# Performance work log

Hardware: AMD Instinct MI355X
Metric: run time of the kernel (lower is better)

## Reference

```python
import jax, jax.numpy as jnp
import numpy as np

N_HEADS = 8
N_NODES = 100_000
DEG = 16
N_EDGES = N_NODES * DEG
IN_DIM = 256
OUT_DIM = 128


def setup_inputs() -> dict:
    key = jax.random.key(0)
    k1, k2, k3, k4 = jax.random.split(key, 4)
    X = jax.random.normal(k1, (N_NODES, IN_DIM), dtype=jnp.float32)
    weights = jax.random.normal(k2, (IN_DIM, OUT_DIM), dtype=jnp.float32) * (1.0 / np.sqrt(IN_DIM))
    attention_w = jax.random.normal(k3, (1, N_HEADS), dtype=jnp.float32) * 0.1
    # valid CSR with uniform degree DEG
    row_pointers = (jnp.arange(N_NODES + 1, dtype=jnp.int32) * DEG)
    column_index = jax.random.randint(k4, (N_EDGES,), 0, N_NODES, dtype=jnp.int32)
    # TC-GNN block bookkeeping tensors: kernel-schedule metadata, no effect on math
    blockPartition = jnp.zeros(((N_NODES + 15) // 16,), dtype=jnp.int32)
    edgeToColumn = jnp.zeros((N_EDGES,), dtype=jnp.int32)
    edgeToRow = jnp.zeros((N_EDGES,), dtype=jnp.int32)
    return {
        "X": X,
        "weights": weights,
        "attention_w": attention_w,
        "row_pointers": row_pointers,
        "column_index": column_index,
        "blockPartition": blockPartition,
        "edgeToColumn": edgeToColumn,
        "edgeToRow": edgeToRow,
    }


def reference(X, weights, attention_w, row_pointers, column_index,
              blockPartition, edgeToColumn, edgeToRow):
    n_nodes = X.shape[0]
    n_edges = column_index.shape[0]
    # dense projection: X_prime = X @ W  -> [n_nodes, out_dim]
    X_prime = X @ weights
    # CSR row id of each edge: row_ids[e] = r s.t. row_pointers[r] <= e < row_pointers[r+1]
    row_ids = jnp.searchsorted(row_pointers,
                               jnp.arange(n_edges, dtype=row_pointers.dtype),
                               side="right") - 1
    # SDDMM (GAcc.forward_ef): per-edge scalar feature = <X_prime[src], X_prime[dst]>
    dst = X_prime[column_index]                    # [E, out_dim]
    edge_feature = jnp.sum(X_prime[row_ids] * dst, axis=-1)  # [E]
    # edge_attentions = outer(edge_feature, attention_w) -> [n_heads, E];
    # aggregation kernel collapses heads: att_e = edge_feature_e * sum_h(w_h)
    att = edge_feature * jnp.sum(attention_w)      # [E]
    # attention-weighted SpMM (GAcc.forward_gat): scatter-add into destination rows
    out = jax.ops.segment_sum(att[:, None] * dst, row_ids, num_segments=n_nodes)
    return out
```

## Files before the change

kernel.cpp:

```cpp
#include <hip/hip_runtime.h>
#include <hip/hip_bf16.h>
#include <stdint.h>

#define N_NODES 100000
#define IN_DIM 256
#define OUT_DIM 128
#define DEG 16

typedef __bf16 bf16x8 __attribute__((ext_vector_type(8)));
typedef __bf16 bf16x4 __attribute__((ext_vector_type(4)));
typedef float f32x4 __attribute__((ext_vector_type(4)));

__global__ void prep_w_kernel(const float* __restrict__ W, __bf16* __restrict__ Wt) {
    const int j = blockIdx.x;
    const int k = threadIdx.x;
    Wt[j * IN_DIM + k] = (__bf16)W[k * OUT_DIM + j];
}

__global__ __launch_bounds__(256) void gemm_kernel(const float* __restrict__ X,
                                                   const __bf16* __restrict__ Wt,
                                                   __bf16* __restrict__ XP) {
    __shared__ __bf16 Alds[32][264];
    const int m0 = blockIdx.x * 32;
    const int t = threadIdx.x;

    {
        const int row = t >> 3;
        const int seg = (t & 7) * 32;
        const float* src = X + (size_t)(m0 + row) * IN_DIM + seg;
        #pragma unroll
        for (int i = 0; i < 8; ++i) {
            float4 v = *reinterpret_cast<const float4*>(src + i * 4);
            bf16x4 b;
            b[0] = (__bf16)v.x; b[1] = (__bf16)v.y; b[2] = (__bf16)v.z; b[3] = (__bf16)v.w;
            *reinterpret_cast<bf16x4*>(&Alds[row][seg + i * 4]) = b;
        }
    }
    __syncthreads();

    const int lane = t & 63;
    const int wave = t >> 6;
    const int n0 = wave * 32;
    const int lr = lane & 15;
    const int lg = lane >> 4;
    f32x4 acc[2][2] = {};

    const __bf16* wbase0 = Wt + (size_t)(n0 + lr) * IN_DIM;
    const __bf16* wbase1 = Wt + (size_t)(n0 + 16 + lr) * IN_DIM;

    #pragma unroll
    for (int kk = 0; kk < IN_DIM; kk += 32) {
        const int ko = kk + lg * 8;
        bf16x8 a0 = *reinterpret_cast<const bf16x8*>(&Alds[lr][ko]);
        bf16x8 a1 = *reinterpret_cast<const bf16x8*>(&Alds[16 + lr][ko]);
        bf16x8 b0 = *reinterpret_cast<const bf16x8*>(wbase0 + ko);
        bf16x8 b1 = *reinterpret_cast<const bf16x8*>(wbase1 + ko);
        acc[0][0] = __builtin_amdgcn_mfma_f32_16x16x32_bf16(a0, b0, acc[0][0], 0, 0, 0);
        acc[0][1] = __builtin_amdgcn_mfma_f32_16x16x32_bf16(a0, b1, acc[0][1], 0, 0, 0);
        acc[1][0] = __builtin_amdgcn_mfma_f32_16x16x32_bf16(a1, b0, acc[1][0], 0, 0, 0);
        acc[1][1] = __builtin_amdgcn_mfma_f32_16x16x32_bf16(a1, b1, acc[1][1], 0, 0, 0);
    }

    #pragma unroll
    for (int mi = 0; mi < 2; ++mi)
        #pragma unroll
        for (int ni = 0; ni < 2; ++ni)
            #pragma unroll
            for (int r = 0; r < 4; ++r) {
                const int row = m0 + mi * 16 + lg * 4 + r;
                const int col = n0 + ni * 16 + lr;
                XP[(size_t)row * OUT_DIM + col] = (__bf16)acc[mi][ni][r];
            }
}

__global__ __launch_bounds__(256) void gat_edge_kernel(const __bf16* __restrict__ XP,
                                                       const int* __restrict__ rp,
                                                       const int* __restrict__ ci,
                                                       const float* __restrict__ attw,
                                                       float* __restrict__ out) {
    const int lane = threadIdx.x & 63;
    const int row = blockIdx.x * 4 + (threadIdx.x >> 6);
    const int g = lane >> 4;
    const int sl = lane & 15;

    float s = 0.f;
    #pragma unroll
    for (int h = 0; h < 8; ++h) s += attw[h];

    float x[8];
    {
        uint4 xv = *reinterpret_cast<const uint4*>(XP + (size_t)row * OUT_DIM + sl * 8);
        const uint32_t* xw = reinterpret_cast<const uint32_t*>(&xv);
        #pragma unroll
        for (int i = 0; i < 4; ++i) {
            x[2 * i]     = __uint_as_float(xw[i] << 16);
            x[2 * i + 1] = __uint_as_float(xw[i] & 0xffff0000u);
        }
    }

    const int4 cv = reinterpret_cast<const int4*>(ci + (size_t)row * DEG)[g];
    const int c[4] = {cv.x, cv.y, cv.z, cv.w};

    uint4 dvu[4];
    #pragma unroll
    for (int j = 0; j < 4; ++j)
        dvu[j] = *reinterpret_cast<const uint4*>(XP + (size_t)c[j] * OUT_DIM + sl * 8);

    float d[4][8];
    #pragma unroll
    for (int j = 0; j < 4; ++j) {
        const uint32_t* dw = reinterpret_cast<const uint32_t*>(&dvu[j]);
        #pragma unroll
        for (int i = 0; i < 4; ++i) {
            d[j][2 * i]     = __uint_as_float(dw[i] << 16);
            d[j][2 * i + 1] = __uint_as_float(dw[i] & 0xffff0000u);
        }
    }

    float p[4];
    #pragma unroll
    for (int j = 0; j < 4; ++j) {
        float t0 = 0.f;
        #pragma unroll
        for (int i = 0; i < 8; ++i) t0 += x[i] * d[j][i];
        p[j] = t0;
    }
    #pragma unroll
    for (int off = 1; off <= 8; off <<= 1) {
        #pragma unroll
        for (int j = 0; j < 4; ++j) p[j] += __shfl_xor(p[j], off);
    }

    float acc[8] = {};
    #pragma unroll
    for (int j = 0; j < 4; ++j) {
        const float att = p[j] * s;
        #pragma unroll
        for (int i = 0; i < 8; ++i) acc[i] += att * d[j][i];
    }

    #pragma unroll
    for (int off = 16; off <= 32; off <<= 1) {
        #pragma unroll
        for (int i = 0; i < 8; ++i) acc[i] += __shfl_xor(acc[i], off);
    }

    if (g == 0) {
        float4 o0, o1;
        o0.x = acc[0]; o0.y = acc[1]; o0.z = acc[2]; o0.w = acc[3];
        o1.x = acc[4]; o1.y = acc[5]; o1.z = acc[6]; o1.w = acc[7];
        float* dst = out + (size_t)row * OUT_DIM + sl * 8;
        *reinterpret_cast<float4*>(dst) = o0;
        *reinterpret_cast<float4*>(dst + 4) = o1;
    }
}

extern "C" void kernel_launch(void* const* d_in, const int* in_sizes, int n_in,
                              void* d_out, int out_size, void* d_ws, size_t ws_size,
                              hipStream_t stream) {
    const float* X    = (const float*)d_in[0];
    const float* W    = (const float*)d_in[1];
    const float* attw = (const float*)d_in[2];
    const int*   rp   = (const int*)d_in[3];
    const int*   ci   = (const int*)d_in[4];
    float* out = (float*)d_out;

    __bf16* XP = (__bf16*)d_ws;
    __bf16* Wt = (__bf16*)((char*)d_ws + (size_t)N_NODES * OUT_DIM * 2);

    prep_w_kernel<<<OUT_DIM, IN_DIM, 0, stream>>>(W, Wt);
    gemm_kernel<<<N_NODES / 32, 256, 0, stream>>>(X, Wt, XP);
    gat_edge_kernel<<<N_NODES / 4, 256, 0, stream>>>(XP, rp, ci, attw, out);
}
```

Baseline: 108.4 us.

## Give each wave a full 32x128 GEMM tile, loading X directly without LDS

The GEMM now has each wave compute all 128 output columns for its own 32 rows. It reads fp32 X straight from global memory into registers, converts to bf16 there, and drops the shared-memory staging and barrier. Before, four waves shared one 32-row tile staged through LDS. The aim is to remove LDS traffic and the sync and to raise MFMA work per load. The cost is 64 accumulator registers per lane, which may lower occupancy, and each wave re-reading all of W from cache.

```diff
diff --git a/kernel.cpp b/kernel.cpp
--- a/kernel.cpp
+++ b/kernel.cpp
@@ -8,7 +8,6 @@
 #define DEG 16
 
 typedef __bf16 bf16x8 __attribute__((ext_vector_type(8)));
-typedef __bf16 bf16x4 __attribute__((ext_vector_type(4)));
 typedef float f32x4 __attribute__((ext_vector_type(4)));
 
 __global__ void prep_w_kernel(const float* __restrict__ W, __bf16* __restrict__ Wt) {
@@ -20,55 +19,53 @@
 __global__ __launch_bounds__(256) void gemm_kernel(const float* __restrict__ X,
                                                    const __bf16* __restrict__ Wt,
                                                    __bf16* __restrict__ XP) {
-    __shared__ __bf16 Alds[32][264];
-    const int m0 = blockIdx.x * 32;
     const int t = threadIdx.x;
-
-    {
-        const int row = t >> 3;
-        const int seg = (t & 7) * 32;
-        const float* src = X + (size_t)(m0 + row) * IN_DIM + seg;
-        #pragma unroll
-        for (int i = 0; i < 8; ++i) {
-            float4 v = *reinterpret_cast<const float4*>(src + i * 4);
-            bf16x4 b;
-            b[0] = (__bf16)v.x; b[1] = (__bf16)v.y; b[2] = (__bf16)v.z; b[3] = (__bf16)v.w;
-            *reinterpret_cast<bf16x4*>(&Alds[row][seg + i * 4]) = b;
-        }
-    }
-    __syncthreads();
-
     const int lane = t & 63;
-    const int wave = t >> 6;
-    const int n0 = wave * 32;
+    const int wid = blockIdx.x * 4 + (t >> 6);
+    const int m0 = wid * 32;
+    if (m0 >= N_NODES) return;
     const int lr = lane & 15;
     const int lg = lane >> 4;
-    f32x4 acc[2][2] = {};
 
-    const __bf16* wbase0 = Wt + (size_t)(n0 + lr) * IN_DIM;
-    const __bf16* wbase1 = Wt + (size_t)(n0 + 16 + lr) * IN_DIM;
+    f32x4 acc[2][8] = {};
+
+    const float*  a0p = X  + (size_t)(m0 + lr) * IN_DIM + lg * 8;
+    const float*  a1p = a0p + (size_t)16 * IN_DIM;
+    const __bf16* bp  = Wt + (size_t)lr * IN_DIM + lg * 8;
 
     #pragma unroll
-    for (int kk = 0; kk < IN_DIM; kk += 32) {
-        const int ko = kk + lg * 8;
-        bf16x8 a0 = *reinterpret_cast<const bf16x8*>(&Alds[lr][ko]);
-        bf16x8 a1 = *reinterpret_cast<const bf16x8*>(&Alds[16 + lr][ko]);
-        bf16x8 b0 = *reinterpret_cast<const bf16x8*>(wbase0 + ko);
-        bf16x8 b1 = *reinterpret_cast<const bf16x8*>(wbase1 + ko);
-        acc[0][0] = __builtin_amdgcn_mfma_f32_16x16x32_bf16(a0, b0, acc[0][0], 0, 0, 0);
-        acc[0][1] = __builtin_amdgcn_mfma_f32_16x16x32_bf16(a0, b1, acc[0][1], 0, 0, 0);
-        acc[1][0] = __builtin_amdgcn_mfma_f32_16x16x32_bf16(a1, b0, acc[1][0], 0, 0, 0);
-        acc[1][1] = __builtin_amdgcn_mfma_f32_16x16x32_bf16(a1, b1, acc[1][1], 0, 0, 0);
+    for (int ks = 0; ks < 8; ++ks) {
+        const int ko = ks * 32;
+        float4 av00 = *reinterpret_cast<const float4*>(a0p + ko);
+        float4 av01 = *reinterpret_cast<const float4*>(a0p + ko + 4);
+        float4 av10 = *reinterpret_cast<const float4*>(a1p + ko);
+        float4 av11 = *reinterpret_cast<const float4*>(a1p + ko + 4);
+        bf16x8 b[8];
+        #pragma unroll
+        for (int ni = 0; ni < 8; ++ni)
+            b[ni] = *reinterpret_cast<const bf16x8*>(bp + (size_t)ni * 16 * IN_DIM + ko);
+
+        bf16x8 a0, a1;
+        a0[0] = (__bf16)av00.x; a0[1] = (__bf16)av00.y; a0[2] = (__bf16)av00.z; a0[3] = (__bf16)av00.w;
+        a0[4] = (__bf16)av01.x; a0[5] = (__bf16)av01.y; a0[6] = (__bf16)av01.z; a0[7] = (__bf16)av01.w;
+        a1[0] = (__bf16)av10.x; a1[1] = (__bf16)av10.y; a1[2] = (__bf16)av10.z; a1[3] = (__bf16)av10.w;
+        a1[4] = (__bf16)av11.x; a1[5] = (__bf16)av11.y; a1[6] = (__bf16)av11.z; a1[7] = (__bf16)av11.w;
+
+        #pragma unroll
+        for (int ni = 0; ni < 8; ++ni) {
+            acc[0][ni] = __builtin_amdgcn_mfma_f32_16x16x32_bf16(a0, b[ni], acc[0][ni], 0, 0, 0);
+            acc[1][ni] = __builtin_amdgcn_mfma_f32_16x16x32_bf16(a1, b[ni], acc[1][ni], 0, 0, 0);
+        }
     }
 
     #pragma unroll
     for (int mi = 0; mi < 2; ++mi)
         #pragma unroll
-        for (int ni = 0; ni < 2; ++ni)
+        for (int ni = 0; ni < 8; ++ni)
             #pragma unroll
             for (int r = 0; r < 4; ++r) {
                 const int row = m0 + mi * 16 + lg * 4 + r;
-                const int col = n0 + ni * 16 + lr;
+                const int col = ni * 16 + lr;
                 XP[(size_t)row * OUT_DIM + col] = (__bf16)acc[mi][ni][r];
             }
 }
@@ -169,6 +166,6 @@
     __bf16* Wt = (__bf16*)((char*)d_ws + (size_t)N_NODES * OUT_DIM * 2);
 
     prep_w_kernel<<<OUT_DIM, IN_DIM, 0, stream>>>(W, Wt);
-    gemm_kernel<<<N_NODES / 32, 256, 0, stream>>>(X, Wt, XP);
+    gemm_kernel<<<(3125 + 3) / 4, 256, 0, stream>>>(X, Wt, XP);
     gat_edge_kernel<<<N_NODES / 4, 256, 0, stream>>>(XP, rp, ci, attw, out);
 }
```

New measurement: 116.7 us. 1.08x slower.
